# Kernel tuning notes

Measured on AMD Instinct MI355X. Metric: run time of the kernel, lower is better.

The kernel has to match this reference:

```python
import jax, jax.numpy as jnp
import numpy as np

N = 50000; FIN = 64; H = 128; E = 800000; T = 8
P = 250000; D = 500000; G = 20000; V = 2000; O = 2


def _mp(h, Ws, Wn, b, edge_src, edge_dst, n):
    # mean-aggregation message passing: relu(h Ws + mean_neigh(h) Wn + b)
    deg = jax.ops.segment_sum(jnp.ones(edge_dst.shape[0], h.dtype), edge_dst, n)
    agg = jax.ops.segment_sum(h[edge_src], edge_dst, n) / jnp.maximum(deg, 1.0)[:, None]
    return jax.nn.relu(h @ Ws + agg @ Wn + b)


def _forward(x, W_enc_self, W_enc_nei, b_enc, W2_self, W2_nei, b2, Wd1, bd1, Wd2, bd2,
             counts, edge_src, edge_dst, place_idx, src_idx, t_idx, dst_nodes, dst_seg,
             group_id, variant_of_group):
    n = x.shape[0]
    p = place_idx.shape[0]
    g = variant_of_group.shape[0]
    v = counts.shape[0]
    # first encoder, then T sequential second_encoder applications (feature generations)
    h0 = _mp(x, W_enc_self, W_enc_nei, b_enc, edge_src, edge_dst, n)

    def step(h, _):
        h2 = _mp(h, W2_self, W2_nei, b2, edge_src, edge_dst, n)
        return h2, h2

    _, hs = jax.lax.scan(step, h0, None, length=T)
    feats = jnp.concatenate([h0[None], hs], axis=0)  # [T+1, N, H]

    # gather (place, src) features at the generation index of each prediction
    place_f = feats[t_idx, place_idx]                 # [P, H]
    src_f = feats[t_idx, src_idx]                     # [P, H]
    # dst feature = sum over the destination set of each prediction
    dst_f = jax.ops.segment_sum(feats[t_idx[dst_seg], dst_nodes], dst_seg, p)  # [P, H]

    cat = jnp.concatenate([place_f, src_f, dst_f], axis=-1)  # [P, 3H]
    logits = jax.nn.relu(cat @ Wd1 + bd1) @ Wd2 + bd2        # [P, O]
    logprob = jax.nn.log_softmax(logits, axis=-1)            # [P, O]

    # prev_prob: inclusive running sum of per-step logprob sums within each variant
    group_sums = jax.ops.segment_sum(logprob, group_id, g)   # [G, O]
    cum = jnp.cumsum(group_sums, axis=0)
    var_tot = jax.ops.segment_sum(group_sums, variant_of_group, v)
    var_excl = jnp.cumsum(var_tot, axis=0) - var_tot
    within = cum - var_excl[variant_of_group]                # [G, O]
    prev = within[group_id]                                  # [P, O]

    logc = jnp.log(counts / jnp.sum(counts))                 # log(count/total) per variant
    add = logprob + prev + logc[variant_of_group[group_id]][:, None]
    return jnp.zeros((n, logits.shape[-1]), x.dtype).at[place_idx].add(add)


def setup_inputs() -> dict:
    ks = jax.random.split(jax.random.key(0), 24)
    s = jnp.float32(0.05)
    f32 = jnp.float32
    i32 = jnp.int32
    return {
        "x": jax.random.normal(ks[0], (N, FIN), f32),
        "W_enc_self": jax.random.normal(ks[1], (FIN, H), f32) * s,
        "W_enc_nei": jax.random.normal(ks[2], (FIN, H), f32) * s,
        "b_enc": jax.random.normal(ks[3], (H,), f32) * s,
        "W2_self": jax.random.normal(ks[4], (H, H), f32) * s,
        "W2_nei": jax.random.normal(ks[5], (H, H), f32) * s,
        "b2": jax.random.normal(ks[6], (H,), f32) * s,
        "Wd1": jax.random.normal(ks[7], (3 * H, 3 * H), f32) * s,
        "bd1": jax.random.normal(ks[8], (3 * H,), f32) * s,
        "Wd2": jax.random.normal(ks[9], (3 * H, O), f32) * s,
        "bd2": jax.random.normal(ks[10], (O,), f32) * s,
        "counts": jax.random.uniform(ks[11], (V,), f32) + 0.5,
        "edge_src": jax.random.randint(ks[12], (E,), 0, N, i32),
        "edge_dst": jax.random.randint(ks[13], (E,), 0, N, i32),
        "place_idx": jax.random.randint(ks[14], (P,), 0, N, i32),
        "src_idx": jax.random.randint(ks[15], (P,), 0, N, i32),
        "t_idx": jax.random.randint(ks[16], (P,), 0, T + 1, i32),
        "dst_nodes": jax.random.randint(ks[17], (D,), 0, N, i32),
        "dst_seg": jnp.sort(jax.random.randint(ks[18], (D,), 0, P, i32)),
        "group_id": jnp.sort(jax.random.randint(ks[19], (P,), 0, G, i32)),
        "variant_of_group": jnp.sort(jax.random.randint(ks[20], (G,), 0, V, i32)),
    }


def reference(x, W_enc_self, W_enc_nei, b_enc, W2_self, W2_nei, b2, Wd1, bd1, Wd2, bd2,
              counts, edge_src, edge_dst, place_idx, src_idx, t_idx, dst_nodes, dst_seg,
              group_id, variant_of_group):
    return _forward(x, W_enc_self, W_enc_nei, b_enc, W2_self, W2_nei, b2, Wd1, bd1, Wd2, bd2,
                    counts, edge_src, edge_dst, place_idx, src_idx, t_idx, dst_nodes, dst_seg,
                    group_id, variant_of_group)
```

## Files before the change

### kernel.cpp

```cpp
#include <hip/hip_runtime.h>
#include <math.h>

#define NN 50000
#define FINN 64
#define HD 128
#define EE 800000
#define TT 8
#define PP 250000
#define DD 500000
#define GG 20000
#define VV 2000
#define OO 2

#define DEC_GRID 256
#define DEC_TILES ((PP + 63) / 64)

typedef short short8 __attribute__((ext_vector_type(8)));
typedef float f32x4 __attribute__((ext_vector_type(4)));
typedef unsigned int uint2v __attribute__((ext_vector_type(2)));
typedef unsigned int uint4v __attribute__((ext_vector_type(4)));

__device__ __forceinline__ unsigned short f2bf(float f) {
    unsigned int u = __float_as_uint(f);
    u += 0x7fffu + ((u >> 16) & 1u);
    return (unsigned short)(u >> 16);
}
__device__ __forceinline__ float bf2f(unsigned short u) {
    return __uint_as_float(((unsigned int)u) << 16);
}

__device__ __forceinline__ unsigned char q8(float f) {
    unsigned short u = f2bf(f);
    unsigned int e = (u >> 7) & 0xffu;
    unsigned int s = (u >> 8) & 0x80u;
    if (e < 121u) return (unsigned char)s;
    unsigned int m = u & 0x7fu;
    unsigned int m3 = m >> 4, rr = m & 0xfu;
    m3 += (rr > 8u) || (rr == 8u && (m3 & 1u));
    unsigned int ee = e - 120u;
    if (m3 == 8u) { m3 = 0u; ++ee; }
    if (ee > 15u || (ee == 15u && m3 == 7u)) { ee = 15u; m3 = 6u; }
    return (unsigned char)(s | (ee << 3) | m3);
}
__device__ __forceinline__ unsigned int dq1(unsigned int b) {
    unsigned int t = b & 0x7fu;
    unsigned int r = ((b & 0x80u) << 8) | ((t << 4) + 0x3C00u);
    return t ? r : 0u;
}

#if __has_builtin(__builtin_amdgcn_cvt_pk_f32_fp8)
typedef float float2v __attribute__((ext_vector_type(2)));
__device__ __forceinline__ void acc_u32(float* acc, unsigned int w) {
    float2v lo = __builtin_amdgcn_cvt_pk_f32_fp8(w, false);
    float2v hi = __builtin_amdgcn_cvt_pk_f32_fp8(w, true);
    acc[0] += lo[0]; acc[1] += lo[1]; acc[2] += hi[0]; acc[3] += hi[1];
}
#else
__device__ __forceinline__ void acc_u32(float* acc, unsigned int w) {
    acc[0] += bf2f((unsigned short)dq1(w & 0xffu));
    acc[1] += bf2f((unsigned short)dq1((w >> 8) & 0xffu));
    acc[2] += bf2f((unsigned short)dq1((w >> 16) & 0xffu));
    acc[3] += bf2f((unsigned short)dq1((w >> 24) & 0xffu));
}
#endif

struct us8 { unsigned short v[8]; };

__device__ __forceinline__ void gload_lds16(const void* g, void* l) {
    __builtin_amdgcn_global_load_lds((__attribute__((address_space(1))) void*)g,
                                     (__attribute__((address_space(3))) void*)l, 16, 0, 0);
}

__global__ void count_k(const int* __restrict__ idx, int* __restrict__ counts, int n) {
    int i = blockIdx.x * blockDim.x + threadIdx.x;
    if (i < n) atomicAdd(&counts[idx[i]], 1);
}

__global__ void blk_sum_k(const int* __restrict__ counts, int n, int* __restrict__ bsum) {
    __shared__ int buf[256];
    int t = threadIdx.x, i = blockIdx.x * 256 + t;
    buf[t] = (i < n) ? counts[i] : 0;
    __syncthreads();
    for (int off = 128; off > 0; off >>= 1) {
        if (t < off) buf[t] += buf[t + off];
        __syncthreads();
    }
    if (t == 0) bsum[blockIdx.x] = buf[0];
}

__global__ void scan_small_k(const int* __restrict__ bsum, int nb, int* __restrict__ boff) {
    __shared__ int buf[256];
    int t = threadIdx.x;
    int v = (t < nb) ? bsum[t] : 0;
    buf[t] = v;
    __syncthreads();
    for (int off = 1; off < 256; off <<= 1) {
        int u = (t >= off) ? buf[t - off] : 0;
        __syncthreads();
        buf[t] += u;
        __syncthreads();
    }
    if (t < nb) boff[t] = buf[t] - v;
}

__global__ void rowptr_fill_k(const int* __restrict__ counts, const int* __restrict__ boff,
                              int n, int* __restrict__ rowptr, int total) {
    __shared__ int buf[256];
    int t = threadIdx.x, i = blockIdx.x * 256 + t;
    int v = (i < n) ? counts[i] : 0;
    buf[t] = v;
    __syncthreads();
    for (int off = 1; off < 256; off <<= 1) {
        int u = (t >= off) ? buf[t - off] : 0;
        __syncthreads();
        buf[t] += u;
        __syncthreads();
    }
    if (i < n) rowptr[i] = boff[blockIdx.x] + buf[t] - v;
    if (i == 0) rowptr[n] = total;
}

__global__ void lb_rowptr_k(const int* __restrict__ arr, int n, int* __restrict__ rowptr, int m) {
    int i = blockIdx.x * blockDim.x + threadIdx.x;
    if (i > m) return;
    int lo = 0, hi = n;
    while (lo < hi) {
        int mid = (lo + hi) >> 1;
        if (arr[mid] < i) lo = mid + 1; else hi = mid;
    }
    rowptr[i] = lo;
}

__global__ void fill_csr_k(const int* __restrict__ esrc, const int* __restrict__ edst,
                           const int* __restrict__ rowptr, int* __restrict__ cursor,
                           int* __restrict__ outi, int n) {
    int e = blockIdx.x * blockDim.x + threadIdx.x;
    if (e < n) {
        int d = edst[e];
        int pos = atomicAdd(&cursor[d], 1);
        outi[rowptr[d] + pos] = esrc[e];
    }
}

__global__ void hist9_k(const int* __restrict__ t_idx, int* __restrict__ hist) {
    __shared__ int l[9];
    if (threadIdx.x < 9) l[threadIdx.x] = 0;
    __syncthreads();
    int p = blockIdx.x * 256 + threadIdx.x;
    if (p < PP) atomicAdd(&l[t_idx[p]], 1);
    __syncthreads();
    if (threadIdx.x < 9) atomicAdd(&hist[threadIdx.x], l[threadIdx.x]);
}

__global__ void scan9_k(const int* __restrict__ hist, int* __restrict__ boff9) {
    if (threadIdx.x == 0) {
        int a = 0;
        for (int i = 0; i < 9; ++i) { boff9[i] = a; a += hist[i]; }
        boff9[9] = a;
    }
}

__global__ void bucket_perm_k(const int* __restrict__ t_idx, const int* __restrict__ boff9,
                              int* __restrict__ cursor9, int* __restrict__ pperm) {
    __shared__ int lcnt[9];
    __shared__ int lbase[9];
    int tid = threadIdx.x;
    int p = blockIdx.x * 256 + tid;
    if (tid < 9) lcnt[tid] = 0;
    __syncthreads();
    int t = 0, lr = 0;
    bool ok = p < PP;
    if (ok) {
        t = t_idx[p];
        lr = atomicAdd(&lcnt[t], 1);
    }
    __syncthreads();
    if (tid < 9) lbase[tid] = atomicAdd(&cursor9[tid], lcnt[tid]);
    __syncthreads();
    if (ok) pperm[boff9[t] + lbase[t] + lr] = p;
}

__global__ void prep_k(const float* __restrict__ x,
                       const float* __restrict__ Wes, const float* __restrict__ Wen,
                       const float* __restrict__ W2s, const float* __restrict__ W2n,
                       const float* __restrict__ Wd1,
                       unsigned short* __restrict__ xb, unsigned char* __restrict__ xbq,
                       unsigned short* __restrict__ wenc_t,
                       unsigned short* __restrict__ w2_t, unsigned short* __restrict__ wd1t,
                       unsigned char* __restrict__ wd1tq) {
    int i = blockIdx.x * 256 + threadIdx.x;
    if (i < NN * FINN) {
        float v = x[i];
        xb[i] = f2bf(v);
        xbq[i] = q8(v);
    }
    if (i < HD * 2 * FINN) {
        int c = i / (2 * FINN), k = i - c * (2 * FINN);
        wenc_t[i] = f2bf((k < FINN) ? Wes[k * HD + c] : Wen[(k - FINN) * HD + c]);
    }
    if (i < HD * 2 * HD) {
        int c = i / (2 * HD), k = i - c * (2 * HD);
        w2_t[i] = f2bf((k < HD) ? W2s[k * HD + c] : W2n[(k - HD) * HD + c]);
    }
    if (i < 384 * 384) {
        int n = i / 384, k = i - n * 384;
        float v = Wd1[k * 384 + n];
        wd1t[i] = f2bf(v);
        wd1tq[i] = q8(v);
    }
}

template <int KIN>
__launch_bounds__(256)
__global__ void mpf2_k(const unsigned short* __restrict__ hin,
                       const unsigned char* __restrict__ hinq,
                       const int* __restrict__ rowptr, const int* __restrict__ csr_src,
                       const unsigned short* __restrict__ Wt, const float* __restrict__ bias,
                       unsigned short* __restrict__ hout, unsigned char* __restrict__ houtq) {
    constexpr int CPL = KIN / 64;
    __shared__ unsigned short sm[32 * KIN];
    int tid = threadIdx.x;
    int r = tid >> 3;
    int sl = tid & 7;
    int node = blockIdx.x * 32 + r;
    int rx = r & 7;

    if (node < NN) {
        int s = rowptr[node], e = rowptr[node + 1];
        float acc[8 * CPL] = {};
        int i = s, iB = s + 1;
        int srcA = (i < e) ? csr_src[i] : 0;
        int srcB = (iB < e) ? csr_src[iB] : 0;
        while (i < e) {
            bool hB = iB < e;
            uint4v vA, vB;
            uint2v wA, wB;
            if constexpr (CPL == 2) {
                vA = *(const uint4v*)&hinq[(size_t)srcA * KIN + sl * 16];
                if (hB) vB = *(const uint4v*)&hinq[(size_t)srcB * KIN + sl * 16];
            } else {
                wA = *(const uint2v*)&hinq[(size_t)srcA * KIN + sl * 8];
                if (hB) wB = *(const uint2v*)&hinq[(size_t)srcB * KIN + sl * 8];
            }
            int iN = i + 2, iN2 = i + 3;
            srcA = (iN < e) ? csr_src[iN] : 0;
            srcB = (iN2 < e) ? csr_src[iN2] : 0;
            if constexpr (CPL == 2) {
                acc_u32(acc + 0, vA[0]); acc_u32(acc + 4, vA[1]);
                acc_u32(acc + 8, vA[2]); acc_u32(acc + 12, vA[3]);
                if (hB) {
                    acc_u32(acc + 0, vB[0]); acc_u32(acc + 4, vB[1]);
                    acc_u32(acc + 8, vB[2]); acc_u32(acc + 12, vB[3]);
                }
            } else {
                acc_u32(acc + 0, wA[0]); acc_u32(acc + 4, wA[1]);
                if (hB) { acc_u32(acc + 0, wB[0]); acc_u32(acc + 4, wB[1]); }
            }
            i = iN; iB = iN2;
        }
        float d = fmaxf((float)(e - s), 1.f);
        us8 o0, o1;
#pragma unroll
        for (int j = 0; j < 8; ++j) o0.v[j] = f2bf(acc[j] / d);
        int c0 = sl * CPL;
        *(us8*)&sm[r * KIN + ((c0 ^ rx) * 8)] = o0;
        if constexpr (CPL == 2) {
#pragma unroll
            for (int j = 0; j < 8; ++j) o1.v[j] = f2bf(acc[8 + j] / d);
            *(us8*)&sm[r * KIN + (((c0 + 1) ^ rx) * 8)] = o1;
        }
    }
    __syncthreads();

    int lane = tid & 63, w = tid >> 6;
    int cc = lane & 15, gq = lane >> 4;
    constexpr int K = 2 * KIN;
    int rloc = (w & 1) * 16 + cc;
    int rowA = blockIdx.x * 32 + rloc;
    bool rowok = rowA < NN;
    const unsigned short* hrow = hin + (size_t)rowA * KIN;
    int ch = (w >> 1) * 64;
    int rlx = rloc & 7;

    f32x4 acc2[4];
#pragma unroll
    for (int t = 0; t < 4; ++t) acc2[t] = (f32x4){0.f, 0.f, 0.f, 0.f};

#pragma unroll
    for (int k0 = 0; k0 < K; k0 += 32) {
        int k = k0 + gq * 8;
        short8 a = {0, 0, 0, 0, 0, 0, 0, 0};
        if (rowok) {
            if (k0 < KIN) a = *(const short8*)(hrow + k);
            else {
                int chunk = (k - KIN) >> 3;
                a = *(const short8*)&sm[rloc * KIN + ((chunk ^ rlx) * 8)];
            }
        }
#pragma unroll
        for (int t = 0; t < 4; ++t) {
            short8 b = *(const short8*)&Wt[(size_t)(ch + t * 16 + cc) * K + k];
            acc2[t] = __builtin_amdgcn_mfma_f32_16x16x32_bf16(a, b, acc2[t], 0, 0, 0);
        }
    }
#pragma unroll
    for (int t = 0; t < 4; ++t) {
        int col = ch + t * 16 + cc;
        float b1 = bias[col];
#pragma unroll
        for (int rj = 0; rj < 4; ++rj) {
            int grow = blockIdx.x * 32 + (w & 1) * 16 + gq * 4 + rj;
            if (grow < NN) {
                float v = fmaxf(acc2[t][rj] + b1, 0.f);
                hout[(size_t)grow * HD + col] = f2bf(v);
                houtq[(size_t)grow * HD + col] = q8(v);
            }
        }
    }
}

__launch_bounds__(256)
__global__ void dst_sum2q_k(const unsigned char* __restrict__ featsq,
                            const int* __restrict__ t_idx, const int* __restrict__ dst_nodes,
                            const int* __restrict__ dst_rowptr, const int* __restrict__ pperm,
                            unsigned char* __restrict__ dstcq) {
    int tid = threadIdx.x;
    int grp = tid >> 4;
    int fl = tid & 15;
    int pi = blockIdx.x * 16 + grp;
    if (pi >= PP) return;
    int p = pperm[pi];
    long t = t_idx[p];
    const unsigned char* base = featsq + (size_t)t * NN * HD;
    int s = dst_rowptr[p], e = dst_rowptr[p + 1];
    float acc[8] = {};
    int i = s;
    int n0 = (i < e) ? dst_nodes[i] : 0;
    int n1 = (i + 1 < e) ? dst_nodes[i + 1] : 0;
    while (i < e) {
        bool h1 = (i + 1) < e;
        uint2v v0 = *(const uint2v*)&base[(size_t)n0 * HD + fl * 8];
        uint2v v1;
        if (h1) v1 = *(const uint2v*)&base[(size_t)n1 * HD + fl * 8];
        int i2 = i + 2, i3 = i + 3;
        n0 = (i2 < e) ? dst_nodes[i2] : 0;
        n1 = (i3 < e) ? dst_nodes[i3] : 0;
        acc_u32(acc + 0, v0[0]); acc_u32(acc + 4, v0[1]);
        if (h1) { acc_u32(acc + 0, v1[0]); acc_u32(acc + 4, v1[1]); }
        i = i2;
    }
    unsigned long long ov = 0;
#pragma unroll
    for (int j = 0; j < 8; ++j) ov |= (unsigned long long)q8(acc[j]) << (8 * j);
    *(unsigned long long*)&dstcq[(size_t)pi * HD + fl * 8] = ov;
}

__global__ void
__attribute__((amdgpu_flat_work_group_size(512, 512), amdgpu_waves_per_eu(2, 2)))
dec11_k(const unsigned char* __restrict__ featsq,
        const unsigned char* __restrict__ dstcq,
        const int* __restrict__ place_idx, const int* __restrict__ src_idx,
        const int* __restrict__ t_idx, const int* __restrict__ group_id,
        const int* __restrict__ pperm,
        const unsigned char* __restrict__ wd1tq,
        const float* __restrict__ bd1, const float* __restrict__ Wd2,
        const float* __restrict__ bd2, float* __restrict__ logprob,
        float* __restrict__ group_sums) {
    __shared__ unsigned char buf[4][192 * 128];
    __shared__ unsigned int rb[4][192];
    __shared__ float lpart[3][8][64][2];

    int tid = threadIdx.x;
    int lane = tid & 63, w = tid >> 6;
    int cc = lane & 15, gq = lane >> 4;
    int bid = blockIdx.x;

    int row = min(tid, 191);
    int sec = row >> 6, pl = row & 63;
    const int* nptr = (sec == 0) ? place_idx : src_idx;
    unsigned int dstc_off = (unsigned int)(dstcq - featsq);

    int nt = (DEC_TILES - 1 - bid) / DEC_GRID + 1;
    float b20 = bd2[0], b21 = bd2[1];

    if (tid < 192) {
#pragma unroll
        for (int s4 = 0; s4 < 4; ++s4) {
            int pic = min((bid + s4 * DEC_GRID) * 64 + pl, PP - 1);
            int p = pperm[pic];
            rb[s4][tid] = (sec == 2) ? (dstc_off + (unsigned int)pic * 128u)
                                     : (unsigned int)(((unsigned)t_idx[p] * NN + (unsigned)nptr[p]) * 128u);
        }
    }
    int p4 = pperm[min((bid + 4 * DEC_GRID) * 64 + pl, PP - 1)];
    int tOld = t_idx[p4], nOld = nptr[p4];
    int pCur = pperm[min((bid + 5 * DEC_GRID) * 64 + pl, PP - 1)];
    int opPP = 0, opP = 0, ogP = 0;

    unsigned long long breg[36];
    float b1r[3], w0r[3], w1r[3];
    {
        const unsigned char* bbase = wd1tq + ((long)(w * 48 + cc) * 384 + gq * 8);
#pragma unroll
        for (int kk = 0; kk < 12; ++kk)
#pragma unroll
            for (int t = 0; t < 3; ++t)
                breg[kk * 3 + t] = *(const unsigned long long*)(bbase + (long)t * 16 * 384 + kk * 32);
#pragma unroll
        for (int t = 0; t < 3; ++t) {
            int col = w * 48 + t * 16 + cc;
            b1r[t] = bd1[col];
            w0r[t] = Wd2[col * 2 + 0];
            w1r[t] = Wd2[col * 2 + 1];
        }
    }
    __syncthreads();

    int rsub8 = lane >> 3, chunk8 = lane & 7;

#define STAGE(slot_)                                                                 \
    {                                                                                \
        _Pragma("unroll")                                                            \
        for (int i = 0; i < 3; ++i) {                                                \
            int r = w * 24 + i * 8 + rsub8;                                          \
            const unsigned char* src = featsq + rb[slot_][r] +                       \
                                       ((unsigned)(chunk8 ^ (r & 7)) << 4);          \
            gload_lds16(src, &buf[slot_][(w * 24 + i * 8) * 128]);                   \
        }                                                                            \
    }

#define OUTPUT(tile_, slot_, opv_, ogv_)                                             \
    {                                                                                \
        int pi = (bid + (tile_) * DEC_GRID) * 64 + w * 16 + cc;                      \
        if (pi < PP) {                                                               \
            float l0 = b20, l1 = b21;                                                \
            _Pragma("unroll")                                                        \
            for (int w2 = 0; w2 < 8; ++w2) {                                         \
                l0 += lpart[slot_][w2][w * 16 + cc][0];                              \
                l1 += lpart[slot_][w2][w * 16 + cc][1];                              \
            }                                                                        \
            float mm = fmaxf(l0, l1);                                                \
            float lse = mm + logf(expf(l0 - mm) + expf(l1 - mm));                    \
            float lp0 = l0 - lse, lp1 = l1 - lse;                                    \
            logprob[(opv_)*2 + 0] = lp0;                                             \
            logprob[(opv_)*2 + 1] = lp1;                                             \
            atomicAdd(&group_sums[(ogv_)*2 + 0], lp0);                               \
            atomicAdd(&group_sums[(ogv_)*2 + 1], lp1);                               \
        }                                                                            \
    }

    STAGE(0);
    STAGE(1);
    STAGE(2);

    for (int k = 0; k < nt; ++k) {
        int slot = k & 3;

        int opN = pperm[min((bid + k * DEC_GRID) * 64 + (w & 3) * 16 + cc, PP - 1)];
        int ogN = group_id[opP];
        int pNew = pperm[min((bid + (k + 6) * DEC_GRID) * 64 + pl, PP - 1)];
        int tNew = t_idx[pCur];
        int nNew = nptr[pCur];
        __builtin_amdgcn_sched_barrier(0);

        if (k + 3 < nt) STAGE((k + 3) & 3);
        __builtin_amdgcn_sched_barrier(0);

        if (k + 3 < nt) {
            if (k >= 2)      { asm volatile("s_waitcnt vmcnt(24)" ::: "memory"); }
            else if (k == 1) { asm volatile("s_waitcnt vmcnt(19)" ::: "memory"); }
            else             { asm volatile("s_waitcnt vmcnt(14)" ::: "memory"); }
        } else if (k + 2 < nt) {
            asm volatile("s_waitcnt vmcnt(21)" ::: "memory");
        } else if (k + 1 < nt) {
            asm volatile("s_waitcnt vmcnt(18)" ::: "memory");
        } else {
            asm volatile("s_waitcnt vmcnt(15)" ::: "memory");
        }
        __builtin_amdgcn_s_barrier();
        __builtin_amdgcn_sched_barrier(0);

        if (k >= 2 && w < 4 && lane < 16) OUTPUT(k - 2, (k - 2) % 3, opPP, ogP);

        {
            const unsigned char* bufc = &buf[slot][0];
            f32x4 acc[4][3];
#pragma unroll
            for (int s = 0; s < 4; ++s)
#pragma unroll
                for (int t = 0; t < 3; ++t) acc[s][t] = (f32x4){0.f, 0.f, 0.f, 0.f};

#pragma unroll
            for (int kk = 0; kk < 12; ++kk) {
                int seck = kk >> 2;
                int eb = (kk & 3) * 32 + gq * 8;
                int c16 = eb >> 4, sub = (eb >> 3) & 1;
                long a_c[4];
#pragma unroll
                for (int s = 0; s < 4; ++s) {
                    int lrow = seck * 64 + s * 16 + cc;
                    a_c[s] = *(const long*)
                        &bufc[lrow * 128 + ((c16 ^ (lrow & 7)) << 4) + sub * 8];
                }
#pragma unroll
                for (int t = 0; t < 3; ++t)
#pragma unroll
                    for (int s = 0; s < 4; ++s)
                        acc[s][t] = __builtin_amdgcn_mfma_f32_16x16x32_fp8_fp8(
                            a_c[s], (long)breg[kk * 3 + t], acc[s][t], 0, 0, 0);
            }

#pragma unroll
            for (int s = 0; s < 4; ++s) {
                float p0[4], p1[4];
#pragma unroll
                for (int r = 0; r < 4; ++r) { p0[r] = 0.f; p1[r] = 0.f; }
#pragma unroll
                for (int t = 0; t < 3; ++t) {
#pragma unroll
                    for (int r = 0; r < 4; ++r) {
                        float h = fmaxf(acc[s][t][r] + b1r[t], 0.f);
                        p0[r] += h * w0r[t];
                        p1[r] += h * w1r[t];
                    }
                }
#pragma unroll
                for (int m = 1; m < 16; m <<= 1)
#pragma unroll
                    for (int r = 0; r < 4; ++r) {
                        p0[r] += __shfl_xor(p0[r], m);
                        p1[r] += __shfl_xor(p1[r], m);
                    }
                if (cc == 0) {
#pragma unroll
                    for (int r = 0; r < 4; ++r) {
                        int orow = s * 16 + gq * 4 + r;
                        lpart[k % 3][w][orow][0] = p0[r];
                        lpart[k % 3][w][orow][1] = p1[r];
                    }
                }
            }
        }

        if (tid < 192) {
            int picw = min((bid + (k + 4) * DEC_GRID) * 64 + pl, PP - 1);
            rb[k & 3][tid] = (sec == 2)
                ? (dstc_off + (unsigned int)picw * 128u)
                : (unsigned int)(((unsigned)tOld * NN + (unsigned)nOld) * 128u);
        }
        tOld = tNew; nOld = nNew; pCur = pNew;
        opPP = opP; opP = opN; ogP = ogN;

        asm volatile("s_waitcnt lgkmcnt(0)" ::: "memory");
        __builtin_amdgcn_s_barrier();
        __builtin_amdgcn_sched_barrier(0);
    }

    if (w < 4 && lane < 16) {
        OUTPUT(nt - 2, (nt - 2) % 3, opPP, ogP);
        int ogLast = group_id[opP];
        OUTPUT(nt - 1, (nt - 1) % 3, opP, ogLast);
    }
#undef STAGE
#undef OUTPUT
}

__global__ void within_total_k(const float* __restrict__ group_sums,
                               const int* __restrict__ var_rowptr,
                               const float* __restrict__ counts,
                               float* __restrict__ within, float* __restrict__ total) {
    __shared__ float buf[256];
    int tid = threadIdx.x;
    float s = 0.f;
    for (int i = tid; i < VV; i += 256) s += counts[i];
    buf[tid] = s;
    __syncthreads();
    for (int off = 128; off > 0; off >>= 1) {
        if (tid < off) buf[tid] += buf[tid + off];
        __syncthreads();
    }
    if (tid == 0) total[0] = buf[0];
    for (int v = tid; v < VV; v += 256) {
        int gs = var_rowptr[v], ge = var_rowptr[v + 1];
        float r0 = 0.f, r1 = 0.f;
        for (int g = gs; g < ge; ++g) {
            r0 += group_sums[2 * g + 0];
            r1 += group_sums[2 * g + 1];
            within[2 * g + 0] = r0;
            within[2 * g + 1] = r1;
        }
    }
}

__global__ void final_k(const float* __restrict__ logprob, const float* __restrict__ within,
                        const int* __restrict__ group_id, const int* __restrict__ vog,
                        const float* __restrict__ counts, const float* __restrict__ total,
                        const int* __restrict__ place_idx, float* __restrict__ outp) {
    int p = blockIdx.x * blockDim.x + threadIdx.x;
    if (p >= PP) return;
    int g = group_id[p];
    int v = vog[g];
    float lc = logf(counts[v]) - logf(total[0]);
    int node = place_idx[p];
    atomicAdd(&outp[node * 2 + 0], logprob[p * 2 + 0] + within[g * 2 + 0] + lc);
    atomicAdd(&outp[node * 2 + 1], logprob[p * 2 + 1] + within[g * 2 + 1] + lc);
}

extern "C" void kernel_launch(void* const* d_in, const int* in_sizes, int n_in,
                              void* d_out, int out_size, void* d_ws, size_t ws_size,
                              hipStream_t stream) {
    const float* x          = (const float*)d_in[0];
    const float* W_enc_self = (const float*)d_in[1];
    const float* W_enc_nei  = (const float*)d_in[2];
    const float* b_enc      = (const float*)d_in[3];
    const float* W2_self    = (const float*)d_in[4];
    const float* W2_nei     = (const float*)d_in[5];
    const float* b2         = (const float*)d_in[6];
    const float* Wd1        = (const float*)d_in[7];
    const float* bd1        = (const float*)d_in[8];
    const float* Wd2        = (const float*)d_in[9];
    const float* bd2        = (const float*)d_in[10];
    const float* counts     = (const float*)d_in[11];
    const int* edge_src     = (const int*)d_in[12];
    const int* edge_dst     = (const int*)d_in[13];
    const int* place_idx    = (const int*)d_in[14];
    const int* src_idx      = (const int*)d_in[15];
    const int* t_idx        = (const int*)d_in[16];
    const int* dst_nodes    = (const int*)d_in[17];
    const int* dst_seg      = (const int*)d_in[18];
    const int* group_id     = (const int*)d_in[19];
    const int* variant_of_group = (const int*)d_in[20];
    float* outp = (float*)d_out;

    const int NB = (NN + 255) / 256;

    unsigned short* rot0 = (unsigned short*)d_ws;
    unsigned short* rot1 = rot0 + (size_t)NN * HD;
    unsigned short* xb   = rot1 + (size_t)NN * HD;
    unsigned char* xbq   = (unsigned char*)(xb + (size_t)NN * FINN);
    unsigned char* featsq = xbq + (size_t)NN * FINN;
    unsigned char* dstcq  = featsq + (size_t)(TT + 1) * NN * HD;
    unsigned short* wenc_t = (unsigned short*)(dstcq + (size_t)PP * HD);
    unsigned short* w2_t   = wenc_t + HD * 2 * FINN;
    unsigned short* wd1t   = w2_t + HD * 2 * HD;
    unsigned char* wd1tq   = (unsigned char*)(wd1t + 384 * 384);
    int* zr = (int*)(wd1tq + 384 * 384);
    int* csr_counts   = zr;
    int* csr_cursor   = csr_counts + NN;
    float* group_sums = (float*)(csr_cursor + NN);
    int* hist9        = (int*)(group_sums + 2 * GG);
    int* cursor9      = hist9 + 9;
    size_t zero_words = (size_t)NN + NN + 2 * GG + 18;
    int* bsum       = cursor9 + 9;
    int* boff       = bsum + 256;
    int* boff9      = boff + 256;
    int* csr_rowptr = boff9 + 16;
    int* dst_rowptr = csr_rowptr + (NN + 1);
    int* var_rowptr = dst_rowptr + (PP + 1);
    int* csr_src    = var_rowptr + (VV + 1);
    int* pperm      = csr_src + EE;
    float* logprob  = (float*)(pperm + PP);
    float* within   = logprob + 2 * PP;
    float* total_counts = within + 2 * GG;

    hipMemsetAsync(zr, 0, zero_words * 4, stream);
    hipMemsetAsync(d_out, 0, (size_t)out_size * sizeof(float), stream);

    prep_k<<<(NN * FINN + 255) / 256, 256, 0, stream>>>(x, W_enc_self, W_enc_nei, W2_self,
                                                        W2_nei, Wd1, xb, xbq, wenc_t, w2_t,
                                                        wd1t, wd1tq);
    count_k<<<(EE + 255) / 256, 256, 0, stream>>>(edge_dst, csr_counts, EE);
    blk_sum_k<<<NB, 256, 0, stream>>>(csr_counts, NN, bsum);
    scan_small_k<<<1, 256, 0, stream>>>(bsum, NB, boff);
    rowptr_fill_k<<<NB, 256, 0, stream>>>(csr_counts, boff, NN, csr_rowptr, EE);
    fill_csr_k<<<(EE + 255) / 256, 256, 0, stream>>>(edge_src, edge_dst, csr_rowptr,
                                                     csr_cursor, csr_src, EE);
    lb_rowptr_k<<<(PP + 256) / 256, 256, 0, stream>>>(dst_seg, DD, dst_rowptr, PP);
    lb_rowptr_k<<<(VV + 256) / 256, 256, 0, stream>>>(variant_of_group, GG, var_rowptr, VV);
    hist9_k<<<(PP + 255) / 256, 256, 0, stream>>>(t_idx, hist9);
    scan9_k<<<1, 64, 0, stream>>>(hist9, boff9);
    bucket_perm_k<<<(PP + 255) / 256, 256, 0, stream>>>(t_idx, boff9, cursor9, pperm);

    const int NB32 = (NN + 31) / 32;
    for (int r = 0; r <= TT; ++r) {
        const unsigned short* hin = (r == 0) ? xb : ((r & 1) ? rot0 : rot1);
        const unsigned char* hinq = (r == 0) ? xbq : featsq + (size_t)(r - 1) * NN * HD;
        unsigned short* hout = (r & 1) ? rot1 : rot0;
        unsigned char* houtq = featsq + (size_t)r * NN * HD;
        if (r == 0)
            mpf2_k<FINN><<<NB32, 256, 0, stream>>>(hin, hinq, csr_rowptr, csr_src, wenc_t,
                                                   b_enc, hout, houtq);
        else
            mpf2_k<HD><<<NB32, 256, 0, stream>>>(hin, hinq, csr_rowptr, csr_src, w2_t,
                                                 b2, hout, houtq);
    }

    dst_sum2q_k<<<(PP + 15) / 16, 256, 0, stream>>>(featsq, t_idx, dst_nodes, dst_rowptr,
                                                    pperm, dstcq);
    dec11_k<<<DEC_GRID, 512, 0, stream>>>(featsq, dstcq, place_idx, src_idx, t_idx,
                                          group_id, pperm, wd1tq, bd1, Wd2, bd2,
                                          logprob, group_sums);

    within_total_k<<<1, 256, 0, stream>>>(group_sums, var_rowptr, counts, within, total_counts);
    final_k<<<(PP + 255) / 256, 256, 0, stream>>>(logprob, within, group_id, variant_of_group,
                                                  counts, total_counts, place_idx, outp);
}
```

Before: 910.2 us.

## Sort nodes by in-degree and predictions by (t, dst count) for load balance

Builds a degree-bucketed node permutation (counting sort on clamped in-degree) and runs every message-passing kernel over nodes in that order, so the 32 nodes handled by a block have similar neighbour counts. The prediction permutation is also refined to bucket by generation index and destination-set size, which evens out per-wave work in the dst-sum and decoder kernels. In exchange, rows are scattered in the GEMM phase (indirect hin reads and hout writes instead of contiguous ones), and there are extra small histogram and scan kernels.

Result: slower. 1.446 ms (+58.9%).

```diff
diff --git a/kernel.cpp b/kernel.cpp
--- a/kernel.cpp
+++ b/kernel.cpp
@@ -142,42 +142,54 @@
     }
 }
 
-__global__ void hist9_k(const int* __restrict__ t_idx, int* __restrict__ hist) {
-    __shared__ int l[9];
-    if (threadIdx.x < 9) l[threadIdx.x] = 0;
+__global__ void scanN_k(const int* __restrict__ hist, int n, int* __restrict__ base) {
+    __shared__ int buf[512];
+    int t = threadIdx.x;
+    int v = (t < n) ? hist[t] : 0;
+    buf[t] = v;
     __syncthreads();
-    int p = blockIdx.x * 256 + threadIdx.x;
-    if (p < PP) atomicAdd(&l[t_idx[p]], 1);
-    __syncthreads();
-    if (threadIdx.x < 9) atomicAdd(&hist[threadIdx.x], l[threadIdx.x]);
-}
-
-__global__ void scan9_k(const int* __restrict__ hist, int* __restrict__ boff9) {
-    if (threadIdx.x == 0) {
-        int a = 0;
-        for (int i = 0; i < 9; ++i) { boff9[i] = a; a += hist[i]; }
-        boff9[9] = a;
-    }
-}
-
-__global__ void bucket_perm_k(const int* __restrict__ t_idx, const int* __restrict__ boff9,
-                              int* __restrict__ cursor9, int* __restrict__ pperm) {
-    __shared__ int lcnt[9];
-    __shared__ int lbase[9];
-    int tid = threadIdx.x;
-    int p = blockIdx.x * 256 + tid;
-    if (tid < 9) lcnt[tid] = 0;
-    __syncthreads();
-    int t = 0, lr = 0;
-    bool ok = p < PP;
-    if (ok) {
-        t = t_idx[p];
-        lr = atomicAdd(&lcnt[t], 1);
-    }
-    __syncthreads();
-    if (tid < 9) lbase[tid] = atomicAdd(&cursor9[tid], lcnt[tid]);
-    __syncthreads();
-    if (ok) pperm[boff9[t] + lbase[t] + lr] = p;
+    for (int off = 1; off < 512; off <<= 1) {
+        int u = (t >= off) ? buf[t - off] : 0;
+        __syncthreads();
+        buf[t] += u;
+        __syncthreads();
+    }
+    if (t < n) base[t] = buf[t] - v;
+}
+
+__global__ void nhist_k(const int* __restrict__ counts, int* __restrict__ nhist) {
+    int i = blockIdx.x * blockDim.x + threadIdx.x;
+    if (i < NN) atomicAdd(&nhist[min(counts[i], 63)], 1);
+}
+
+__global__ void nperm_build_k(const int* __restrict__ counts, const int* __restrict__ nbase,
+                              int* __restrict__ ncur, int* __restrict__ nperm) {
+    int i = blockIdx.x * blockDim.x + threadIdx.x;
+    if (i < NN) {
+        int d = min(counts[i], 63);
+        int pos = nbase[d] + atomicAdd(&ncur[d], 1);
+        nperm[pos] = i;
+    }
+}
+
+__global__ void phist_k(const int* __restrict__ t_idx, const int* __restrict__ dst_rowptr,
+                        int* __restrict__ hist288) {
+    int p = blockIdx.x * blockDim.x + threadIdx.x;
+    if (p < PP) {
+        int key = t_idx[p] * 32 + min(dst_rowptr[p + 1] - dst_rowptr[p], 31);
+        atomicAdd(&hist288[key], 1);
+    }
+}
+
+__global__ void pperm_build_k(const int* __restrict__ t_idx, const int* __restrict__ dst_rowptr,
+                              const int* __restrict__ pbase, int* __restrict__ pcur,
+                              int* __restrict__ pperm) {
+    int p = blockIdx.x * blockDim.x + threadIdx.x;
+    if (p < PP) {
+        int key = t_idx[p] * 32 + min(dst_rowptr[p + 1] - dst_rowptr[p], 31);
+        int pos = pbase[key] + atomicAdd(&pcur[key], 1);
+        pperm[pos] = p;
+    }
 }
 
 __global__ void prep_k(const float* __restrict__ x,
@@ -215,6 +227,7 @@
 __global__ void mpf2_k(const unsigned short* __restrict__ hin,
                        const unsigned char* __restrict__ hinq,
                        const int* __restrict__ rowptr, const int* __restrict__ csr_src,
+                       const int* __restrict__ nperm,
                        const unsigned short* __restrict__ Wt, const float* __restrict__ bias,
                        unsigned short* __restrict__ hout, unsigned char* __restrict__ houtq) {
     constexpr int CPL = KIN / 64;
@@ -222,10 +235,11 @@
     int tid = threadIdx.x;
     int r = tid >> 3;
     int sl = tid & 7;
-    int node = blockIdx.x * 32 + r;
+    int gi = blockIdx.x * 32 + r;
+    int node = (gi < NN) ? nperm[gi] : -1;
     int rx = r & 7;
 
-    if (node < NN) {
+    if (node >= 0) {
         int s = rowptr[node], e = rowptr[node + 1];
         float acc[8 * CPL] = {};
         int i = s, iB = s + 1;
@@ -276,11 +290,22 @@
     int cc = lane & 15, gq = lane >> 4;
     constexpr int K = 2 * KIN;
     int rloc = (w & 1) * 16 + cc;
-    int rowA = blockIdx.x * 32 + rloc;
-    bool rowok = rowA < NN;
-    const unsigned short* hrow = hin + (size_t)rowA * KIN;
+    int gi2 = blockIdx.x * 32 + rloc;
+    bool rowok = gi2 < NN;
+    int nodeB = rowok ? nperm[gi2] : 0;
+    const unsigned short* hrow = hin + (size_t)nodeB * KIN;
     int ch = (w >> 1) * 64;
     int rlx = rloc & 7;
+
+    int gnode[4];
+    {
+        int gbase = blockIdx.x * 32 + (w & 1) * 16 + gq * 4;
+#pragma unroll
+        for (int rj = 0; rj < 4; ++rj) {
+            int growi = gbase + rj;
+            gnode[rj] = (growi < NN) ? nperm[growi] : -1;
+        }
+    }
 
     f32x4 acc2[4];
 #pragma unroll
@@ -309,11 +334,10 @@
         float b1 = bias[col];
 #pragma unroll
         for (int rj = 0; rj < 4; ++rj) {
-            int grow = blockIdx.x * 32 + (w & 1) * 16 + gq * 4 + rj;
-            if (grow < NN) {
+            if (gnode[rj] >= 0) {
                 float v = fmaxf(acc2[t][rj] + b1, 0.f);
-                hout[(size_t)grow * HD + col] = f2bf(v);
-                houtq[(size_t)grow * HD + col] = q8(v);
+                hout[(size_t)gnode[rj] * HD + col] = f2bf(v);
+                houtq[(size_t)gnode[rj] * HD + col] = q8(v);
             }
         }
     }
@@ -648,18 +672,22 @@
     int* csr_counts   = zr;
     int* csr_cursor   = csr_counts + NN;
     float* group_sums = (float*)(csr_cursor + NN);
-    int* hist9        = (int*)(group_sums + 2 * GG);
-    int* cursor9      = hist9 + 9;
-    size_t zero_words = (size_t)NN + NN + 2 * GG + 18;
-    int* bsum       = cursor9 + 9;
+    int* hist288      = (int*)(group_sums + 2 * GG);
+    int* cur288       = hist288 + 288;
+    int* nhist        = cur288 + 288;
+    int* ncur         = nhist + 64;
+    size_t zero_words = (size_t)NN + NN + 2 * GG + 704;
+    int* bsum       = ncur + 64;
     int* boff       = bsum + 256;
-    int* boff9      = boff + 256;
-    int* csr_rowptr = boff9 + 16;
+    int* pbase      = boff + 256;
+    int* nbase      = pbase + 288;
+    int* csr_rowptr = nbase + 64;
     int* dst_rowptr = csr_rowptr + (NN + 1);
     int* var_rowptr = dst_rowptr + (PP + 1);
     int* csr_src    = var_rowptr + (VV + 1);
     int* pperm      = csr_src + EE;
-    float* logprob  = (float*)(pperm + PP);
+    int* nperm      = pperm + PP;
+    float* logprob  = (float*)(nperm + NN);
     float* within   = logprob + 2 * PP;
     float* total_counts = within + 2 * GG;
 
@@ -677,9 +705,14 @@
                                                      csr_cursor, csr_src, EE);
     lb_rowptr_k<<<(PP + 256) / 256, 256, 0, stream>>>(dst_seg, DD, dst_rowptr, PP);
     lb_rowptr_k<<<(VV + 256) / 256, 256, 0, stream>>>(variant_of_group, GG, var_rowptr, VV);
-    hist9_k<<<(PP + 255) / 256, 256, 0, stream>>>(t_idx, hist9);
-    scan9_k<<<1, 64, 0, stream>>>(hist9, boff9);
-    bucket_perm_k<<<(PP + 255) / 256, 256, 0, stream>>>(t_idx, boff9, cursor9, pperm);
+
+    nhist_k<<<NB, 256, 0, stream>>>(csr_counts, nhist);
+    scanN_k<<<1, 512, 0, stream>>>(nhist, 64, nbase);
+    nperm_build_k<<<NB, 256, 0, stream>>>(csr_counts, nbase, ncur, nperm);
+
+    phist_k<<<(PP + 255) / 256, 256, 0, stream>>>(t_idx, dst_rowptr, hist288);
+    scanN_k<<<1, 512, 0, stream>>>(hist288, 288, pbase);
+    pperm_build_k<<<(PP + 255) / 256, 256, 0, stream>>>(t_idx, dst_rowptr, pbase, cur288, pperm);
 
     const int NB32 = (NN + 31) / 32;
     for (int r = 0; r <= TT; ++r) {
@@ -688,11 +721,11 @@
         unsigned short* hout = (r & 1) ? rot1 : rot0;
         unsigned char* houtq = featsq + (size_t)r * NN * HD;
         if (r == 0)
-            mpf2_k<FINN><<<NB32, 256, 0, stream>>>(hin, hinq, csr_rowptr, csr_src, wenc_t,
-                                                   b_enc, hout, houtq);
+            mpf2_k<FINN><<<NB32, 256, 0, stream>>>(hin, hinq, csr_rowptr, csr_src, nperm,
+                                                   wenc_t, b_enc, hout, houtq);
         else
-            mpf2_k<HD><<<NB32, 256, 0, stream>>>(hin, hinq, csr_rowptr, csr_src, w2_t,
-                                                 b2, hout, houtq);
+            mpf2_k<HD><<<NB32, 256, 0, stream>>>(hin, hinq, csr_rowptr, csr_src, nperm,
+                                                 w2_t, b2, hout, houtq);
     }
 
     dst_sum2q_k<<<(PP + 15) / 16, 256, 0, stream>>>(featsq, t_idx, dst_nodes, dst_rowptr,
```
